# Kernel optimization log

Hardware: AMD Instinct MI355X
Metric: run time of the kernel (lower is better)

## Reference

```python
import jax, jax.numpy as jnp
import numpy as np

EPS = 1e-5


def _bn(x, g, b):
    # BatchNorm1d in training mode: batch mean, biased variance, eps=1e-5
    m = jnp.mean(x, axis=0)
    v = jnp.var(x, axis=0)
    return (x - m) * jax.lax.rsqrt(v + EPS) * g + b


def setup_inputs() -> dict:
    key = jax.random.key(0)
    ks = jax.random.split(key, 16)
    B, N, F, H = 4096, 128, 4, 32
    w = lambda k, o, i: jax.random.normal(k, (o, i), jnp.float32) * 0.3
    d = {
        'u': jax.random.normal(ks[0], (B, N, F), jnp.float32),
        'mask': jnp.ones((B * N, 1), jnp.int32),
        # MLPphi params
        'p_bn1_g': jnp.ones((F,), jnp.float32), 'p_bn1_b': jnp.zeros((F,), jnp.float32), 'p_w1': w(ks[1], H, F),
        'p_bn2_g': jnp.ones((H,), jnp.float32), 'p_bn2_b': jnp.zeros((H,), jnp.float32), 'p_w2': w(ks[2], H, H),
        'p_bn3_g': jnp.ones((H,), jnp.float32), 'p_bn3_b': jnp.zeros((H,), jnp.float32), 'p_w3': w(ks[3], H, H),
        # MLPomega params
        'o_bn1_g': jnp.ones((F,), jnp.float32), 'o_bn1_b': jnp.zeros((F,), jnp.float32), 'o_w1': w(ks[4], H, F),
        'o_bn2_g': jnp.ones((H,), jnp.float32), 'o_bn2_b': jnp.zeros((H,), jnp.float32), 'o_w2': w(ks[5], H, H),
        'o_bn3_g': jnp.ones((H,), jnp.float32), 'o_bn3_b': jnp.zeros((H,), jnp.float32), 'o_w3': w(ks[6], H, H),
        # MLPtheta params
        't_bn1_g': jnp.ones((H,), jnp.float32), 't_bn1_b': jnp.zeros((H,), jnp.float32), 't_w1': w(ks[7], H, H),
        't_bn2_g': jnp.ones((H,), jnp.float32), 't_bn2_b': jnp.zeros((H,), jnp.float32), 't_w2': w(ks[8], H, H),
        't_bn3_g': jnp.ones((H,), jnp.float32), 't_bn3_b': jnp.zeros((H,), jnp.float32), 't_w3': w(ks[9], H, H),
        't_bn4_g': jnp.ones((H,), jnp.float32), 't_bn4_b': jnp.zeros((H,), jnp.float32),
        't_w4': w(ks[10], 1, H), 't_b4': jnp.zeros((1,), jnp.float32),
    }
    return d


def _forward(u, mask,
             p_bn1_g, p_bn1_b, p_w1, p_bn2_g, p_bn2_b, p_w2, p_bn3_g, p_bn3_b, p_w3,
             o_bn1_g, o_bn1_b, o_w1, o_bn2_g, o_bn2_b, o_w2, o_bn3_g, o_bn3_b, o_w3,
             t_bn1_g, t_bn1_b, t_w1, t_bn2_g, t_bn2_b, t_w2, t_bn3_g, t_bn3_b, t_w3,
             t_bn4_g, t_bn4_b, t_w4, t_b4):
    B, N, F = u.shape
    H = p_w1.shape[0]
    u_flat = u.reshape(-1, F)  # (B*N, F)

    # MLPphi: three BN+Linear(no bias)+Tanh blocks with residual adds (dropout=identity in eval)
    o1 = jnp.tanh(_bn(u_flat, p_bn1_g, p_bn1_b) @ p_w1.T)
    o2 = jnp.tanh(_bn(o1, p_bn2_g, p_bn2_b) @ p_w2.T)
    o3 = jnp.tanh(_bn(o1 + o2, p_bn3_g, p_bn3_b) @ p_w3.T)
    x_main = (o1 + o2 + o3).reshape(B, N, H)

    # MLPomega: BN+Linear+Tanh x2, BN+Linear, softmax over hidden dim (dim=1 of flat), then masked_fill
    a = jnp.tanh(_bn(u_flat, o_bn1_g, o_bn1_b) @ o_w1.T)
    a = jnp.tanh(_bn(a, o_bn2_g, o_bn2_b) @ o_w2.T)
    a = _bn(a, o_bn3_g, o_bn3_b) @ o_w3.T
    a = jax.nn.softmax(a, axis=1)
    a = jnp.where(mask == 0, -jnp.inf, a)
    x_attn = a.reshape(B, N, H)

    # attention pooling over neighbors
    x = jnp.sum(x_main * x_attn, axis=1)  # (B, H)

    x = jnp.tanh(_bn(x, t_bn1_g, t_bn1_b) @ t_w1.T)
    x = jnp.tanh(_bn(x, t_bn2_g, t_bn2_b) @ t_w2.T)
    x = jnp.tanh(_bn(x, t_bn3_g, t_bn3_b) @ t_w3.T)
    x = _bn(x, t_bn4_g, t_bn4_b) @ t_w4.T + t_b4
    return x


def reference(u, mask,
              p_bn1_g, p_bn1_b, p_w1, p_bn2_g, p_bn2_b, p_w2, p_bn3_g, p_bn3_b, p_w3,
              o_bn1_g, o_bn1_b, o_w1, o_bn2_g, o_bn2_b, o_w2, o_bn3_g, o_bn3_b, o_w3,
              t_bn1_g, t_bn1_b, t_w1, t_bn2_g, t_bn2_b, t_w2, t_bn3_g, t_bn3_b, t_w3,
              t_bn4_g, t_bn4_b, t_w4, t_b4):
    return _forward(u, mask,
                    p_bn1_g, p_bn1_b, p_w1, p_bn2_g, p_bn2_b, p_w2, p_bn3_g, p_bn3_b, p_w3,
                    o_bn1_g, o_bn1_b, o_w1, o_bn2_g, o_bn2_b, o_w2, o_bn3_g, o_bn3_b, o_w3,
                    t_bn1_g, t_bn1_b, t_w1, t_bn2_g, t_bn2_b, t_w2, t_bn3_g, t_bn3_b, t_w3,
                    t_bn4_g, t_bn4_b, t_w4, t_b4)
```

## Files before the change

### kernel.cpp

```cpp
#include <hip/hip_runtime.h>

typedef unsigned int u32;
typedef unsigned short u16;
typedef __attribute__((ext_vector_type(8))) _Float16 half8;
typedef __attribute__((ext_vector_type(4))) float f32x4;

#define ROWS  524288
#define BROWS 4096
#define EPS   1e-5f

#define S_U   0
#define S_O1  8
#define S_A1  72
#define S_O12 136
#define S_A2  200
#define S_X   264
#define S_X1  328
#define S_X2  392
#define S_X3  456
#define SHARD 1024
#define NSH   64

#define XSTR 40

__device__ __forceinline__ float bl(u32 u){ return __uint_as_float(u << 16); }
__device__ __forceinline__ float bh(u32 u){ return __uint_as_float(u & 0xFFFF0000u); }
__device__ __forceinline__ float b2f(u16 h){ return __uint_as_float(((u32)h) << 16); }
__device__ __forceinline__ u16 f2b(float f){
  u32 u = __float_as_uint(f);
  return (u16)((u + 0x7FFFu + ((u >> 16) & 1u)) >> 16);
}
__device__ __forceinline__ u16 f2h(float f){ _Float16 h = (_Float16)f; return __builtin_bit_cast(u16, h); }
__device__ __forceinline__ float h2f(u16 x){ return (float)__builtin_bit_cast(_Float16, x); }
__device__ __forceinline__ u32 pack2h(float a, float b){
  auto v = __builtin_amdgcn_cvt_pkrtz(a, b);
  return __builtin_bit_cast(u32, v);
}
__device__ __forceinline__ float lo16(u32 w){ return h2f((u16)(w & 0xFFFF)); }
__device__ __forceinline__ float hi16(u32 w){ return h2f((u16)(w >> 16)); }
__device__ __forceinline__ void unpk4(uint2 v, float* d){
  d[0]=lo16(v.x); d[1]=hi16(v.x); d[2]=lo16(v.y); d[3]=hi16(v.y);
}

__device__ __forceinline__ float tanh_fast(float x){
  float x2 = x*x;
  float num = fmaf(x2 + 105.0f, x2, 945.0f) * x;
  float den = fmaf(fmaf(x2, 15.0f, 420.0f), x2, 945.0f);
  float v = num * __builtin_amdgcn_rcpf(den);
  return fminf(1.0f, fmaxf(-1.0f, v));
}

template<bool F32>
__device__ __forceinline__ float rdp(const void* p, int i){
  if (F32) return ((const float*)p)[i];
  return b2f(((const u16*)p)[i]);
}
template<bool F32>
__device__ __forceinline__ void load_u4(const void* u, int r, float* f){
  if (F32){
    float4 v = ((const float4*)u)[r];
    f[0]=v.x; f[1]=v.y; f[2]=v.z; f[3]=v.w;
  } else {
    uint2 v = ((const uint2*)u)[r];
    f[0]=bl(v.x); f[1]=bh(v.x); f[2]=bl(v.y); f[3]=bh(v.y);
  }
}

__device__ __forceinline__ int detect_u(const u16* __restrict__ u, int tid, int* sf){
  if (tid < 64){
    int bad = 0;
#pragma unroll
    for (int i = 0; i < 4; ++i){
      int e = (u[tid*4 + i] >> 7) & 0xFF;
      bad += (e >= 0x90) ? 1 : 0;
    }
#pragma unroll
    for (int off = 32; off >= 1; off >>= 1) bad += __shfl_down(bad, off);
    if (tid == 0) *sf = (bad >= 4) ? 1 : 0;
  }
  __syncthreads();
  return *sf;
}

__device__ __forceinline__ void g2lrow(const u16* __restrict__ g, int r, u16* X, int tid){
  const uint4* src = (const uint4*)&g[(size_t)r*32];
  uint4* dst = (uint4*)&X[tid*XSTR];
#pragma unroll
  for (int c=0;c<4;++c) dst[c] = src[c];
}
__device__ __forceinline__ void l2grow(const u16* X, int tid, u16* __restrict__ g, int r){
  const uint4* src = (const uint4*)&X[tid*XSTR];
  uint4* dst = (uint4*)&g[(size_t)r*32];
#pragma unroll
  for (int c=0;c<4;++c) dst[c] = src[c];
}

template<bool F32>
__device__ __forceinline__ void stats_u_body(const void* __restrict__ u, float* __restrict__ S){
  int tid = blockIdx.x*blockDim.x + threadIdx.x;
  int nt  = gridDim.x*blockDim.x;
  float s[4]={0,0,0,0}, q[4]={0,0,0,0};
  for (int r = tid; r < ROWS; r += nt){
    float f[4]; load_u4<F32>(u, r, f);
#pragma unroll
    for (int k=0;k<4;++k){ s[k]+=f[k]; q[k]+=f[k]*f[k]; }
  }
#pragma unroll
  for (int off=32; off>=1; off>>=1){
#pragma unroll
    for (int k=0;k<4;++k){ s[k]+=__shfl_down(s[k],off); q[k]+=__shfl_down(q[k],off); }
  }
  if ((threadIdx.x & 63) == 0){
    float* Sh = S + (blockIdx.x & (NSH-1))*SHARD;
#pragma unroll
    for (int k=0;k<4;++k){ atomicAdd(&Sh[S_U+k], s[k]); atomicAdd(&Sh[S_U+4+k], q[k]); }
  }
}
__global__ __launch_bounds__(256) void k_stats_u(const void* __restrict__ u, float* __restrict__ S){
  __shared__ int sf;
  int isf = detect_u((const u16*)u, threadIdx.x, &sf);
  if (isf) stats_u_body<true>(u,S); else stats_u_body<false>(u,S);
}

__device__ __forceinline__ void prep_u(const float* __restrict__ S, float* mr, int tid){
  if (tid < 4){
    float s=0.f, q=0.f;
    for (int sh=0; sh<NSH; ++sh){
      s += S[sh*SHARD + S_U + tid];
      q += S[sh*SHARD + S_U + 4 + tid];
    }
    float m = s*(1.0f/ROWS);
    float var = q*(1.0f/ROWS) - m*m;
    mr[tid]   = m;
    mr[4+tid] = rsqrtf(var + EPS);
  }
  __syncthreads();
}
template<bool F32>
__device__ __forceinline__ void bn_u_l(const float* mr, const void* g, const void* b,
                                       const float* f, float* xn){
#pragma unroll
  for (int k=0;k<4;++k)
    xn[k] = (f[k]-mr[k])*(rdp<F32>(g,k)*mr[4+k]) + rdp<F32>(b,k);
}

template<bool F32>
__device__ __forceinline__ void chain1_to_lds(const float* xn, const void* W1, u16* Xrow){
// ... 60 lines not shown
__device__ __forceinline__ void mfma_layer(u16* X, const u16* Wt, const float* Cb,
                                           int L, int wv, int lane, const u32* at_pk)
{
  int ln15 = lane & 15, quad = lane >> 4;
  half8 w0 = *(const half8*)&Wt[(L*32 + ln15     )*XSTR + quad*8];
  half8 w1 = *(const half8*)&Wt[(L*32 + ln15 + 16)*XSTR + quad*8];
  float bias0[4], bias1[4];
#pragma unroll
  for (int reg=0;reg<4;++reg){
    bias0[reg] = Cb[L*32 +      quad*4 + reg];
    bias1[reg] = Cb[L*32 + 16 + quad*4 + reg];
  }
  int rowbase = wv*64;
#pragma unroll
  for (int Mt=0; Mt<4; ++Mt){
    int s = rowbase + Mt*16 + ln15;
    half8 bfr = *(const half8*)&X[s*XSTR + quad*8];
    f32x4 c0 = {0.f,0.f,0.f,0.f}, c1 = {0.f,0.f,0.f,0.f};
    c0 = __builtin_amdgcn_mfma_f32_16x16x32_f16(w0, bfr, c0, 0,0,0);
    c1 = __builtin_amdgcn_mfma_f32_16x16x32_f16(w1, bfr, c1, 0,0,0);
    float o0[4], o1v[4];
    if (KIND == KIND_TANHRES || KIND == KIND_TANHRES_ATREG){
      unpk4(*(const uint2*)&X[s*XSTR +      quad*4], o0);
      unpk4(*(const uint2*)&X[s*XSTR + 16 + quad*4], o1v);
    }
    float a0v[4], a1v[4];
    if (KIND == KIND_TANHRES_ATREG){
      a0v[0]=lo16(at_pk[Mt*4+0]); a0v[1]=hi16(at_pk[Mt*4+0]);
      a0v[2]=lo16(at_pk[Mt*4+1]); a0v[3]=hi16(at_pk[Mt*4+1]);
      a1v[0]=lo16(at_pk[Mt*4+2]); a1v[1]=hi16(at_pk[Mt*4+2]);
      a1v[2]=lo16(at_pk[Mt*4+3]); a1v[3]=hi16(at_pk[Mt*4+3]);
    }
    float v0[4], v1[4];
#pragma unroll
    for (int reg=0;reg<4;++reg){
      float a = c0[reg] + bias0[reg];
      float b = c1[reg] + bias1[reg];
      if (KIND == KIND_TANH){ a = tanh_fast(a); b = tanh_fast(b); }
      else if (KIND == KIND_TANHRES){ a = o0[reg] + tanh_fast(a); b = o1v[reg] + tanh_fast(b); }
      else if (KIND == KIND_TANHRES_ATREG){
        a = (o0[reg] + tanh_fast(a)) * a0v[reg];
        b = (o1v[reg] + tanh_fast(b)) * a1v[reg];
      }
      v0[reg] = a; v1[reg] = b;
    }
    uint2 w0o, w1o;
    w0o.x = pack2h(v0[0], v0[1]); w0o.y = pack2h(v0[2], v0[3]);
    w1o.x = pack2h(v1[0], v1[1]); w1o.y = pack2h(v1[2], v1[3]);
    *(uint2*)&X[s*XSTR +      quad*4] = w0o;
    *(uint2*)&X[s*XSTR + 16 + quad*4] = w1o;
  }
}

__device__ __forceinline__ void mfma_logits_softmax(const u16* X, const u16* Wt, const float* Cb,
    int L, int wv, int lane, const int* __restrict__ mask, int maskbase, u32* at_pk)
{
  int ln15 = lane & 15, quad = lane >> 4;
  half8 w0 = *(const half8*)&Wt[(L*32 + ln15     )*XSTR + quad*8];
  half8 w1 = *(const half8*)&Wt[(L*32 + ln15 + 16)*XSTR + quad*8];
  float bias0[4], bias1[4];
#pragma unroll
  for (int reg=0;reg<4;++reg){
    bias0[reg] = Cb[L*32 +      quad*4 + reg];
    bias1[reg] = Cb[L*32 + 16 + quad*4 + reg];
  }
  int rowbase = wv*64;
#pragma unroll
  for (int Mt=0; Mt<4; ++Mt){
    int s = rowbase + Mt*16 + ln15;
    half8 bfr = *(const half8*)&X[s*XSTR + quad*8];
    f32x4 c0 = {0.f,0.f,0.f,0.f}, c1 = {0.f,0.f,0.f,0.f};
    c0 = __builtin_amdgcn_mfma_f32_16x16x32_f16(w0, bfr, c0, 0,0,0);
    c1 = __builtin_amdgcn_mfma_f32_16x16x32_f16(w1, bfr, c1, 0,0,0);
    float l0[4], l1[4];
#pragma unroll
    for (int reg=0;reg<4;++reg){ l0[reg] = c0[reg]+bias0[reg]; l1[reg] = c1[reg]+bias1[reg]; }
    float mx = l0[0];
#pragma unroll
    for (int reg=1;reg<4;++reg) mx = fmaxf(mx, l0[reg]);
#pragma unroll
    for (int reg=0;reg<4;++reg) mx = fmaxf(mx, l1[reg]);
    mx = fmaxf(mx, __shfl_xor(mx, 16));
    mx = fmaxf(mx, __shfl_xor(mx, 32));
    float sum = 0.f;
#pragma unroll
    for (int reg=0;reg<4;++reg){ l0[reg] = __expf(l0[reg]-mx); sum += l0[reg]; }
#pragma unroll
    for (int reg=0;reg<4;++reg){ l1[reg] = __expf(l1[reg]-mx); sum += l1[reg]; }
    sum += __shfl_xor(sum, 16);
    sum += __shfl_xor(sum, 32);
    float inv = __builtin_amdgcn_rcpf(sum);
    bool mz = (mask[maskbase + Mt*16 + ln15] == 0);
#pragma unroll
    for (int reg=0;reg<4;++reg){
      l0[reg] *= inv; l1[reg] *= inv;
      if (mz){ l0[reg] = -__builtin_inff(); l1[reg] = -__builtin_inff(); }
    }
    at_pk[Mt*4+0] = pack2h(l0[0], l0[1]);
    at_pk[Mt*4+1] = pack2h(l0[2], l0[3]);
    at_pk[Mt*4+2] = pack2h(l1[0], l1[1]);
    at_pk[Mt*4+3] = pack2h(l1[2], l1[3]);
  }
}

__device__ __forceinline__ void reduce_f16(const u16* X, float* lds2,
                                           float* __restrict__ S, int offS, int shard)
{
  int tid = threadIdx.x;
  __syncthreads();
  {
    int j = tid & 31, seg = tid >> 5;
    float s=0.f, q=0.f;
    for (int q2=0;q2<32;++q2){
      float v = h2f(X[(seg*32+q2)*XSTR + j]);
      s += v; q = fmaf(v,v,q);
    }
    lds2[seg*32+j] = s;
    lds2[256 + seg*32+j] = q;
  }
  __syncthreads();
  if (tid < 64){
    int j = tid & 31; bool isq = tid >= 32;
    const float* src = lds2 + (isq?256:0);
    float tot=0.f;
#pragma unroll
    for (int sg=0;sg<8;++sg) tot += src[sg*32+j];
    atomicAdd(&S[shard*SHARD + offS + (isq?32:0) + j], tot);
  }
  __syncthreads();
}

__device__ __forceinline__ void reduce_f32(const float* Xs, float* lds2,
                                           float* __restrict__ S, int offS, int shard)
{
  int tid = threadIdx.x;
  __syncthreads();
  {
    int j = tid & 31, seg = tid >> 5;
    float s=0.f, q=0.f;
    for (int q2=0;q2<32;++q2){
      float v = Xs[(seg*32+q2)*33 + j];
      s += v; q = fmaf(v,v,q);
    }
    lds2[seg*32+j] = s;
    lds2[256 + seg*32+j] = q;
  }
  __syncthreads();
  if (tid < 64){
    int j = tid & 31; bool isq = tid >= 32;
    const float* src = lds2 + (isq?256:0);
    float tot=0.f;
#pragma unroll
    for (int sg=0;sg<8;++sg) tot += src[sg*32+j];
    atomicAdd(&S[shard*SHARD + offS + (isq?32:0) + j], tot);
  }
  __syncthreads();
}

template<bool F32>
__device__ __forceinline__ void pass1_body(const void* __restrict__ u,
    const void* pg1, const void* pb1, const void* pw1,
    const void* og1, const void* ob1, const void* ow1,
    float* __restrict__ S, float* Xs, float* lds2, float* mr)
{
  int tid = threadIdx.x;
  int r = blockIdx.x*256 + tid;
  int shard = blockIdx.x & (NSH-1);
  prep_u(S, mr, tid);
  float f[4]; load_u4<F32>(u,r,f);
  float xn[4];
  float* Xp = Xs + tid*33;

  bn_u_l<F32>(mr, pg1, pb1, f, xn);
#pragma unroll
  for (int j=0;j<32;++j)
    Xp[j] = tanh_fast(xn[0]*rdp<F32>(pw1,j*4+0) + xn[1]*rdp<F32>(pw1,j*4+1)
                    + xn[2]*rdp<F32>(pw1,j*4+2) + xn[3]*rdp<F32>(pw1,j*4+3));
  reduce_f32(Xs, lds2, S, S_O1, shard);

  bn_u_l<F32>(mr, og1, ob1, f, xn);
#pragma unroll
  for (int j=0;j<32;++j)
    Xp[j] = tanh_fast(xn[0]*rdp<F32>(ow1,j*4+0) + xn[1]*rdp<F32>(ow1,j*4+1)
                    + xn[2]*rdp<F32>(ow1,j*4+2) + xn[3]*rdp<F32>(ow1,j*4+3));
  reduce_f32(Xs, lds2, S, S_A1, shard);
}
__global__ __launch_bounds__(256) void k_pass1(const void* __restrict__ u,
    const void* pg1, const void* pb1, const void* pw1,
    const void* og1, const void* ob1, const void* ow1,
    float* __restrict__ S){
  __shared__ float Xs[256*33];
  __shared__ float lds2[512];
  __shared__ float mr[8];
  __shared__ int sf;
  int isf = detect_u((const u16*)u, threadIdx.x, &sf);
  if (isf) pass1_body<true >(u,pg1,pb1,pw1,og1,ob1,ow1,S,Xs,lds2,mr);
  else     pass1_body<false>(u,pg1,pb1,pw1,og1,ob1,ow1,S,Xs,lds2,mr);
}

template<bool F32, bool MAT>
__device__ __forceinline__ void pass2_body(const void* __restrict__ u,
    const void* pg1, const void* pb1, const void* pw1,
    const void* og1, const void* ob1, const void* ow1,
    const void* pg2, const void* pb2, const void* pw2,
    const void* og2, const void* ob2, const void* ow2,
    float* __restrict__ S, u16* __restrict__ o12g, u16* __restrict__ a2g,
    u16* X, u16* Wt, float* Cb, float* lds2, float* mr)
{
  int tid = threadIdx.x;
  int wv = tid >> 6, lane = tid & 63;
  int r = blockIdx.x*256 + tid;
  int shard = blockIdx.x & (NSH-1);
  prep_u(S, mr, tid);
  fold2<F32>(S, S_O1, S_A1, pg2,pb2,pw2, og2,ob2,ow2, Wt, Cb, lds2);

  float f[4], xn[4];
  load_u4<F32>(u,r,f);

  bn_u_l<F32>(mr, pg1, pb1, f, xn);
  chain1_to_lds<F32>(xn, pw1, X + tid*XSTR);
  mfma_layer<KIND_TANHRES>(X, Wt, Cb, 0, wv, lane, 0);
  if (MAT) l2grow(X, tid, o12g, r);
  reduce_f16(X, lds2, S, S_O12, shard);

  bn_u_l<F32>(mr, og1, ob1, f, xn);
  chain1_to_lds<F32>(xn, ow1, X + tid*XSTR);
  mfma_layer<KIND_TANH  >(X, Wt, Cb, 1, wv, lane, 0);
  if (MAT) l2grow(X, tid, a2g, r);
  reduce_f16(X, lds2, S, S_A2, shard);
}
template<bool MAT>
__global__ __launch_bounds__(256) void k_pass2(const void* __restrict__ u,
    const void* pg1, const void* pb1, const void* pw1,
    const void* og1, const void* ob1, const void* ow1,
    const void* pg2, const void* pb2, const void* pw2,
    const void* og2, const void* ob2, const void* ow2,
    float* __restrict__ S, u16* o12g, u16* a2g){
  __shared__ u16 X[256*XSTR];
  __shared__ u16 Wt[2*32*XSTR];
  __shared__ float Cb[64];
  __shared__ float lds2[512];
  __shared__ float mr[8];
  __shared__ int sf;
  int isf = detect_u((const u16*)u, threadIdx.x, &sf);
  if (isf) pass2_body<true ,MAT>(u,pg1,pb1,pw1,og1,ob1,ow1,pg2,pb2,pw2,og2,ob2,ow2,S,o12g,a2g,X,Wt,Cb,lds2,mr);
  else     pass2_body<false,MAT>(u,pg1,pb1,pw1,og1,ob1,ow1,pg2,pb2,pw2,og2,ob2,ow2,S,o12g,a2g,X,Wt,Cb,lds2,mr);
}

template<bool F32>
__device__ __forceinline__ void pass3m_body(const int* __restrict__ mask,
    const void* pg3, const void* pb3, const void* pw3,
    const void* og3, const void* ob3, const void* ow3,
    const u16* __restrict__ o12g, const u16* __restrict__ a2g,
    float* __restrict__ x, float* __restrict__ S,
    u16* X, u16* Wt, float* Cb, float* red2)
{
  int tid = threadIdx.x;
  int wv = tid >> 6, lane = tid & 63;
  int r = blockIdx.x*256 + tid;
  fold2<F32>(S, S_A2, S_O12, og3,ob3,ow3, pg3,pb3,pw3, Wt, Cb, red2);

  u32 at_pk[16];
  int maskbase = blockIdx.x*256 + wv*64;

  g2lrow(a2g, r, X, tid);
  __syncthreads();
  mfma_logits_softmax(X, Wt, Cb, 0, wv, lane, mask, maskbase, at_pk);
  __syncthreads();
  g2lrow(o12g, r, X, tid);
  __syncthreads();
  mfma_layer<KIND_TANHRES_ATREG>(X, Wt, Cb, 1, wv, lane, at_pk);

  __syncthreads();
  {
    int jj = tid & 31, cgrp = (tid >> 5) & 3, half = tid >> 7;
    float s2 = 0.f;
    for (int q2=0;q2<32;++q2) s2 += h2f(X[(half*128 + cgrp*32 + q2)*XSTR + jj]);
    red2[tid] = s2;
  }
  __syncthreads();
  if (tid < 64){
    int half = tid >> 5, j = tid & 31;
    float v = red2[half*128+j] + red2[half*128+32+j] + red2[half*128+64+j] + red2[half*128+96+j];
    x[(blockIdx.x*2 + half)*32 + j] = v;
    float* Sh = S + (blockIdx.x & (NSH-1))*SHARD;
    atomicAdd(&Sh[S_X+j], v);
    atomicAdd(&Sh[S_X+32+j], v*v);
  }
}
__global__ __launch_bounds__(256) void k_pass3m(const void* __restrict__ u, const int* __restrict__ mask,
    const void* pg3, const void* pb3, const void* pw3,
    const void* og3, const void* ob3, const void* ow3,
    const u16* o12g, const u16* a2g,
    float* __restrict__ x, float* __restrict__ S){
  __shared__ u16 X [256*XSTR];
  __shared__ u16 Wt[2*32*XSTR];
  __shared__ float Cb[64];
  __shared__ float red2[256];
  __shared__ int sf;
  int isf = detect_u((const u16*)u, threadIdx.x, &sf);
  if (isf) pass3m_body<true >(mask,pg3,pb3,pw3,og3,ob3,ow3,o12g,a2g,x,S,X,Wt,Cb,red2);
  else     pass3m_body<false>(mask,pg3,pb3,pw3,og3,ob3,ow3,o12g,a2g,x,S,X,Wt,Cb,red2);
}

template<bool F32>
__device__ __forceinline__ void fold4(const float* __restrict__ S,
    int off0,int off1,int off2,int off3,
    const void* g0,const void* b0,const void* W0,
    const void* g1,const void* b1,const void* W1,
    const void* g2,const void* b2,const void* W2,
    const void* g3,const void* b3,const void* W3,
    u16* Wt, float* Cb, float* scr)
{
  int tid = threadIdx.x;
  __shared__ float scr2[256];
  if (tid < 128){
    int L = tid>>5, k = tid&31;
    const void* g = (L==0)?g0:(L==1)?g1:(L==2)?g2:g3;
    const void* b = (L==0)?b0:(L==1)?b1:(L==2)?b2:b3;
    int off = (L==0)?off0:(L==1)?off1:(L==2)?off2:off3;
    float s=0.f, q=0.f;
    for (int sh=0; sh<NSH; ++sh){
      s += S[sh*SHARD + off + k];
      q += S[sh*SHARD + off + 32 + k];
    }
    float m    = s*(1.0f/ROWS);
    float var  = q*(1.0f/ROWS) - m*m;
    float rstd = rsqrtf(var+EPS);
    float sc = rdp<F32>(g,k)*rstd;
    scr[tid]  = sc;
    scr2[tid] = rdp<F32>(b,k) - m*sc;
  }
  __syncthreads();
  if (tid < 128){
    int L = tid>>5, j = tid&31;
    const void* W = (L==0)?W0:(L==1)?W1:(L==2)?W2:W3;
    float c = 0.f;
#pragma unroll
    for (int k=0;k<32;++k){
      float Wv = rdp<F32>(W, j*32+k);
      Wt[(L*32+j)*XSTR + k] = f2h(Wv * scr[(L<<5)|k]);
      c += Wv * scr2[(L<<5)|k];
    }
    Cb[L*32+j] = c;
  }
  __syncthreads();
}

template<bool F32>
__device__ __forceinline__ void pass3_body(const void* __restrict__ u, const int* __restrict__ mask,
    const void* pg1, const void* pb1, const void* pw1,
    const void* og1, const void* ob1, const void* ow1,
    const void* pg2, const void* pb2, const void* pw2,
    const void* og2, const void* ob2, const void* ow2,
    const void* pg3, const void* pb3, const void* pw3,
    const void* og3, const void* ob3, const void* ow3,
    float* __restrict__ x, float* __restrict__ S,
    u16* X, u16* Wt, float* Cb, float* red2, float* mr)
{
  int tid = threadIdx.x;
  int wv = tid >> 6, lane = tid & 63;
  int r = blockIdx.x*256 + tid;
  prep_u(S, mr, tid);
  fold4<F32>(S, S_A1, S_A2, S_O1, S_O12,
             og2,ob2,ow2, og3,ob3,ow3, pg2,pb2,pw2, pg3,pb3,pw3,
             Wt, Cb, red2);

  float f[4], xn[4];
  load_u4<F32>(u,r,f);
  u32 at_pk[16];
  int maskbase = blockIdx.x*256 + wv*64;

  bn_u_l<F32>(mr, og1, ob1, f, xn);
  chain1_to_lds<F32>(xn, ow1, X + tid*XSTR);
  mfma_layer<KIND_TANH>(X, Wt, Cb, 0, wv, lane, 0);
  mfma_logits_softmax(X, Wt, Cb, 1, wv, lane, mask, maskbase, at_pk);

  bn_u_l<F32>(mr, pg1, pb1, f, xn);
  chain1_to_lds<F32>(xn, pw1, X + tid*XSTR);
  mfma_layer<KIND_TANHRES   >(X, Wt, Cb, 2, wv, lane, 0);
  mfma_layer<KIND_TANHRES_ATREG>(X, Wt, Cb, 3, wv, lane, at_pk);

  __syncthreads();
  {
    int jj = tid & 31, cgrp = (tid >> 5) & 3, half = tid >> 7;
    float s2 = 0.f;
    for (int q2=0;q2<32;++q2) s2 += h2f(X[(half*128 + cgrp*32 + q2)*XSTR + jj]);
    red2[tid] = s2;
  }
  __syncthreads();
  if (tid < 64){
    int half = tid >> 5, j = tid & 31;
    float v = red2[half*128+j] + red2[half*128+32+j] + red2[half*128+64+j] + red2[half*128+96+j];
    x[(blockIdx.x*2 + half)*32 + j] = v;
    float* Sh = S + (blockIdx.x & (NSH-1))*SHARD;
    atomicAdd(&Sh[S_X+j], v);
    atomicAdd(&Sh[S_X+32+j], v*v);
  }
}
__global__ __launch_bounds__(256) void k_pass3(const void* __restrict__ u, const int* __restrict__ mask,
    const void* pg1, const void* pb1, const void* pw1,
    const void* og1, const void* ob1, const void* ow1,
    const void* pg2, const void* pb2, const void* pw2,
    const void* og2, const void* ob2, const void* ow2,
    const void* pg3, const void* pb3, const void* pw3,
    const void* og3, const void* ob3, const void* ow3,
    float* __restrict__ x, float* __restrict__ S){
  __shared__ u16 X [256*XSTR];
  __shared__ u16 Wt[4*32*XSTR];
  __shared__ float Cb[128];
  __shared__ float red2[256];
  __shared__ float mr[8];
  __shared__ int sf;
  int isf = detect_u((const u16*)u, threadIdx.x, &sf);
  if (isf) pass3_body<true >(u,mask,pg1,pb1,pw1,og1,ob1,ow1,pg2,pb2,pw2,og2,ob2,ow2,
                             pg3,pb3,pw3,og3,ob3,ow3,x,S,X,Wt,Cb,red2,mr);
  else     pass3_body<false>(u,mask,pg1,pb1,pw1,og1,ob1,ow1,pg2,pb2,pw2,og2,ob2,ow2,
                             pg3,pb3,pw3,og3,ob3,ow3,x,S,X,Wt,Cb,red2,mr);
}


template<int NSH_IN>
__device__ __forceinline__ void theta_gather(const float* __restrict__ S, int off,
                                             float* scratch, float* lds2, int tid){
  int col = tid & 63, grp = tid >> 6;
  float t = 0.f;
#pragma unroll
  for (int i = 0; i < NSH_IN/4; ++i)
    t += S[(grp + i*4)*SHARD + off + col];
  scratch[tid] = t;
  __syncthreads();
  if (tid < 64)
    scratch[tid] = scratch[tid] + scratch[64+tid] + scratch[128+tid] + scratch[192+tid];
  __syncthreads();
  if (tid < 32){
    float m   = scratch[tid]*(1.0f/BROWS);
    float var = scratch[32+tid]*(1.0f/BROWS) - m*m;
    lds2[tid]    = m;
    lds2[32+tid] = rsqrtf(var + EPS);
  }
  __syncthreads();
}

template<bool F32>
__device__ __forceinline__ void theta_layer(float* v, const float* lds2,
    const void* g, const void* b, const void* W){
  float xn[32];
#pragma unroll
  for (int k=0;k<32;++k)
    xn[k] = (v[k] - lds2[k]) * (rdp<F32>(g,k)*lds2[32+k]) + rdp<F32>(b,k);
#pragma unroll
  for (int j=0;j<32;++j){
    float acc = 0.f;
#pragma unroll
    for (int k=0;k<32;++k) acc = fmaf(rdp<F32>(W, j*32+k), xn[k], acc);
    v[j] = tanh_fast(acc);
  }
}

template<bool F32, int NSH_IN>
__device__ __forceinline__ void theta_L_body(const float* __restrict__ xin,
    float* __restrict__ xout, float* __restrict__ S, int off_in, int off_out,
    const void* g, const void* b, const void* W, float* lds, float* lds2)
{
  int tid = threadIdx.x, blk = blockIdx.x;
  int r = blk*256 + tid;
  theta_gather<NSH_IN>(S, off_in, lds, lds2, tid);
  float v[32];
  {
    const float4* xr = (const float4*)&xin[(size_t)r*32];
#pragma unroll
    for (int k=0;k<8;++k){ float4 t = xr[k]; v[4*k]=t.x; v[4*k+1]=t.y; v[4*k+2]=t.z; v[4*k+3]=t.w; }
  }
  theta_layer<F32>(v, lds2, g, b, W);
  {
    float4* xw = (float4*)&xout[(size_t)r*32];
#pragma unroll
    for (int k=0;k<8;++k){ float4 t; t.x=v[4*k]; t.y=v[4*k+1]; t.z=v[4*k+2]; t.w=v[4*k+3]; xw[k]=t; }
  }
  float* Xp = lds + tid*33;
#pragma unroll
  for (int j=0;j<32;++j) Xp[j] = v[j];
  reduce_f32(lds, lds2, S, off_out, blk);
}
template<int NSH_IN>
__global__ __launch_bounds__(256) void k_theta_L(const void* __restrict__ u,
    const float* __restrict__ xin, float* __restrict__ xout,
    float* __restrict__ S, int off_in, int off_out,
    const void* g, const void* b, const void* W){
  __shared__ float lds[256*33];
  __shared__ float lds2[512];
  __shared__ int sf;
  int isf = detect_u((const u16*)u, threadIdx.x, &sf);
  if (isf) theta_L_body<true , NSH_IN>(xin, xout, S, off_in, off_out, g, b, W, lds, lds2);
  else     theta_L_body<false, NSH_IN>(xin, xout, S, off_in, off_out, g, b, W, lds, lds2);
}

template<bool F32>
__device__ __forceinline__ void theta_fin_body(const float* __restrict__ xin,
    float* __restrict__ S,
    const void* g4, const void* b4, const void* w4, const void* bb4,
    void* out, float* lds, float* lds2)
{
  int tid = threadIdx.x, blk = blockIdx.x;
  int r = blk*256 + tid;
  theta_gather<16>(S, S_X3, lds, lds2, tid);
  float acc = rdp<F32>(bb4, 0);
  const float4* xr = (const float4*)&xin[(size_t)r*32];
#pragma unroll
  for (int k8=0;k8<8;++k8){
    float4 t = xr[k8];
    float vv[4] = {t.x, t.y, t.z, t.w};
#pragma unroll
    for (int q=0;q<4;++q){
      int k = k8*4+q;
      float xnv = (vv[q] - lds2[k]) * (rdp<F32>(g4,k)*lds2[32+k]) + rdp<F32>(b4,k);
      acc = fmaf(rdp<F32>(w4,k), xnv, acc);
    }
  }
  if (F32) ((float*)out)[r] = acc;
  else     ((u16*)out)[r]  = f2b(acc);
}
__global__ __launch_bounds__(256) void k_theta_fin(const void* __restrict__ u,
    const float* __restrict__ xin, float* __restrict__ S,
    const void* g4, const void* b4, const void* w4, const void* bb4,
    void* out){
  __shared__ float lds[256];
  __shared__ float lds2[512];
  __shared__ int sf;
  int isf = detect_u((const u16*)u, threadIdx.x, &sf);
  if (isf) theta_fin_body<true >(xin, S, g4, b4, w4, bb4, out, lds, lds2);
  else     theta_fin_body<false>(xin, S, g4, b4, w4, bb4, out, lds, lds2);
}

extern "C" void kernel_launch(void* const* d_in, const int* in_sizes, int n_in,
                              void* d_out, int out_size, void* d_ws, size_t ws_size,
                              hipStream_t stream)
{
  const void* u    = d_in[0];
  const int*  mask = (const int*)d_in[1];
  const void *pg1=d_in[2],  *pb1=d_in[3],  *pw1=d_in[4];
  const void *pg2=d_in[5],  *pb2=d_in[6],  *pw2=d_in[7];
  const void *pg3=d_in[8],  *pb3=d_in[9],  *pw3=d_in[10];
  const void *og1=d_in[11], *ob1=d_in[12], *ow1=d_in[13];
  const void *og2=d_in[14], *ob2=d_in[15], *ow2=d_in[16];
  const void *og3=d_in[17], *ob3=d_in[18], *ow3=d_in[19];
  const void *tg1=d_in[20], *tb1=d_in[21], *tw1=d_in[22];
  const void *tg2=d_in[23], *tb2=d_in[24], *tw2=d_in[25];
  const void *tg3=d_in[26], *tb3=d_in[27], *tw3=d_in[28];
  const void *tg4=d_in[29], *tb4=d_in[30], *tw4=d_in[31], *tbb4=d_in[32];

  char* ws = (char*)d_ws;
  float* S    = (float*)(ws + 4096);
  float* x    = (float*)(ws + 524288);
  float* xb   = (float*)(ws + 1048576);

  const size_t MB = 1024*1024;
  u16* o12g = (u16*)(ws + 8*MB);
  u16* a2g  = (u16*)(ws + 40*MB);
  bool MAT = ws_size >= 73*MB;

  (void)hipMemsetAsync(ws, 0, 4096 + NSH*SHARD*4, stream);
  k_stats_u<<<1024, 256, 0, stream>>>(u, S);
  k_pass1<<<2048, 256, 0, stream>>>(u, pg1,pb1,pw1, og1,ob1,ow1, S);
  if (MAT){
    k_pass2<true ><<<2048, 256, 0, stream>>>(u, pg1,pb1,pw1, og1,ob1,ow1,
                                             pg2,pb2,pw2, og2,ob2,ow2, S, o12g, a2g);
    k_pass3m<<<2048, 256, 0, stream>>>(u, mask, pg3,pb3,pw3, og3,ob3,ow3, o12g, a2g, x, S);
  } else {
    k_pass2<false><<<2048, 256, 0, stream>>>(u, pg1,pb1,pw1, og1,ob1,ow1,
                                             pg2,pb2,pw2, og2,ob2,ow2, S, o12g, a2g);
    k_pass3<<<2048, 256, 0, stream>>>(u, mask, pg1,pb1,pw1, og1,ob1,ow1,
                                      pg2,pb2,pw2, og2,ob2,ow2,
                                      pg3,pb3,pw3, og3,ob3,ow3, x, S);
  }
  k_theta_L<64><<<16, 256, 0, stream>>>(u, x,  xb, S, S_X,  S_X1, tg1, tb1, tw1);
  k_theta_L<16><<<16, 256, 0, stream>>>(u, xb, x,  S, S_X1, S_X2, tg2, tb2, tw2);
  k_theta_L<16><<<16, 256, 0, stream>>>(u, x,  xb, S, S_X2, S_X3, tg3, tb3, tw3);
  k_theta_fin<<<16, 256, 0, stream>>>(u, xb, S, tg4, tb4, tw4, tbb4, d_out);
}
```

Before: 318.5 us.

## Compute BN stats in MFMA registers, read pass3 from global, fuse final theta

Pass2 now computes per-column sums and sums of squares straight from the MFMA output registers. It reduces them with cross-lane shuffles and writes activations directly to global memory, replacing the LDS round trip and the strided column reduction. Pass3m feeds MFMA B fragments straight from global o12g/a2g and does the attention pooling in registers, dropping the LDS staging and several barriers. Pass1 now uses the f16 chain1 helper and f16 reduction. The final theta layer is merged into the third theta kernel through a last-block atomic counter, saving one launch at the cost of a serial 16-row tail in a single block.

```diff
diff --git a/kernel.cpp b/kernel.cpp
--- a/kernel.cpp
+++ b/kernel.cpp
@@ -50,6 +50,14 @@
   return fminf(1.0f, fmaxf(-1.0f, v));
 }
 
+__device__ __forceinline__ float red16(float v){
+  v += __shfl_xor(v, 1);
+  v += __shfl_xor(v, 2);
+  v += __shfl_xor(v, 4);
+  v += __shfl_xor(v, 8);
+  return v;
+}
+
 template<bool F32>
 __device__ __forceinline__ float rdp(const void* p, int i){
   if (F32) return ((const float*)p)[i];
@@ -80,19 +88,6 @@
   }
   __syncthreads();
   return *sf;
-}
-
-__device__ __forceinline__ void g2lrow(const u16* __restrict__ g, int r, u16* X, int tid){
-  const uint4* src = (const uint4*)&g[(size_t)r*32];
-  uint4* dst = (uint4*)&X[tid*XSTR];
-#pragma unroll
-  for (int c=0;c<4;++c) dst[c] = src[c];
-}
-__device__ __forceinline__ void l2grow(const u16* X, int tid, u16* __restrict__ g, int r){
-  const uint4* src = (const uint4*)&X[tid*XSTR];
-  uint4* dst = (uint4*)&g[(size_t)r*32];
-#pragma unroll
-  for (int c=0;c<4;++c) dst[c] = src[c];
 }
 
 template<bool F32>
@@ -259,8 +254,9 @@
   }
 }
 
-__device__ __forceinline__ void mfma_logits_softmax(const u16* X, const u16* Wt, const float* Cb,
-    int L, int wv, int lane, const int* __restrict__ mask, int maskbase, u32* at_pk)
+template<int KIND, bool STORE>
+__device__ __forceinline__ void mfma_stat(const u16* X, const u16* Wt, const float* Cb,
+    int L, int wv, int lane, u16* __restrict__ G, int gbase, float* s8, float* q8)
 {
   int ln15 = lane & 15, quad = lane >> 4;
   half8 w0 = *(const half8*)&Wt[(L*32 + ln15     )*XSTR + quad*8];
@@ -271,6 +267,8 @@
     bias0[reg] = Cb[L*32 +      quad*4 + reg];
     bias1[reg] = Cb[L*32 + 16 + quad*4 + reg];
   }
+#pragma unroll
+  for (int i=0;i<8;++i){ s8[i]=0.f; q8[i]=0.f; }
   int rowbase = wv*64;
 #pragma unroll
   for (int Mt=0; Mt<4; ++Mt){
@@ -279,6 +277,79 @@
     f32x4 c0 = {0.f,0.f,0.f,0.f}, c1 = {0.f,0.f,0.f,0.f};
     c0 = __builtin_amdgcn_mfma_f32_16x16x32_f16(w0, bfr, c0, 0,0,0);
     c1 = __builtin_amdgcn_mfma_f32_16x16x32_f16(w1, bfr, c1, 0,0,0);
+    float o0[4], o1v[4];
+    if (KIND == KIND_TANHRES){
+      unpk4(*(const uint2*)&X[s*XSTR +      quad*4], o0);
+      unpk4(*(const uint2*)&X[s*XSTR + 16 + quad*4], o1v);
+    }
+    float v0[4], v1[4];
+#pragma unroll
+    for (int reg=0;reg<4;++reg){
+      float a = c0[reg] + bias0[reg];
+      float b = c1[reg] + bias1[reg];
+      if (KIND == KIND_TANH){ a = tanh_fast(a); b = tanh_fast(b); }
+      else { a = o0[reg] + tanh_fast(a); b = o1v[reg] + tanh_fast(b); }
+      s8[reg]   += a; q8[reg]   = fmaf(a,a,q8[reg]);
+      s8[4+reg] += b; q8[4+reg] = fmaf(b,b,q8[4+reg]);
+      v0[reg] = a; v1[reg] = b;
+    }
+    if (STORE){
+      uint2 w0o, w1o;
+      w0o.x = pack2h(v0[0], v0[1]); w0o.y = pack2h(v0[2], v0[3]);
+      w1o.x = pack2h(v1[0], v1[1]); w1o.y = pack2h(v1[2], v1[3]);
+      size_t R = (size_t)(gbase + s);
+      *(uint2*)&G[R*32 +      quad*4] = w0o;
+      *(uint2*)&G[R*32 + 16 + quad*4] = w1o;
+    }
+  }
+}
+
+__device__ __forceinline__ void emit_stats(float* s8, float* q8, int tid, int wv,
+    int quad, int ln15, float* scr , float* __restrict__ S, int offS, int shard)
+{
+#pragma unroll
+  for (int i=0;i<8;++i){ s8[i]=red16(s8[i]); q8[i]=red16(q8[i]); }
+  __syncthreads();
+  if (ln15 == 0){
+#pragma unroll
+    for (int rg=0; rg<4; ++rg){
+      int cl = quad*4+rg, ch = 16+quad*4+rg;
+      scr[wv*64 + cl]       = s8[rg];
+      scr[wv*64 + ch]       = s8[4+rg];
+      scr[256 + wv*64 + cl] = q8[rg];
+      scr[256 + wv*64 + ch] = q8[4+rg];
+    }
+  }
+  __syncthreads();
+  if (tid < 64){
+    int j = tid & 31, isq = tid >> 5;
+    const float* src = scr + isq*256;
+    float tot = src[j] + src[64+j] + src[128+j] + src[192+j];
+    atomicAdd(&S[shard*SHARD + offS + isq*32 + j], tot);
+  }
+}
+
+__device__ __forceinline__ void mfma_logits_softmax_g(const u16* __restrict__ Gsrc, int gbase,
+    const u16* Wt, const float* Cb, int L, int wv, int lane,
+    const int* __restrict__ mask, int maskbase, u32* at_pk)
+{
+  int ln15 = lane & 15, quad = lane >> 4;
+  half8 w0 = *(const half8*)&Wt[(L*32 + ln15     )*XSTR + quad*8];
+  half8 w1 = *(const half8*)&Wt[(L*32 + ln15 + 16)*XSTR + quad*8];
+  float bias0[4], bias1[4];
+#pragma unroll
+  for (int reg=0;reg<4;++reg){
+    bias0[reg] = Cb[L*32 +      quad*4 + reg];
+    bias1[reg] = Cb[L*32 + 16 + quad*4 + reg];
+  }
+  int rowbase = wv*64;
+#pragma unroll
+  for (int Mt=0; Mt<4; ++Mt){
+    int R = gbase + rowbase + Mt*16 + ln15;
+    half8 bfr = *(const half8*)&Gsrc[(size_t)R*32 + quad*8];
+    f32x4 c0 = {0.f,0.f,0.f,0.f}, c1 = {0.f,0.f,0.f,0.f};
+    c0 = __builtin_amdgcn_mfma_f32_16x16x32_f16(w0, bfr, c0, 0,0,0);
+    c1 = __builtin_amdgcn_mfma_f32_16x16x32_f16(w1, bfr, c1, 0,0,0);
     float l0[4], l1[4];
 #pragma unroll
     for (int reg=0;reg<4;++reg){ l0[reg] = c0[reg]+bias0[reg]; l1[reg] = c1[reg]+bias1[reg]; }
@@ -307,6 +378,46 @@
     at_pk[Mt*4+1] = pack2h(l0[2], l0[3]);
     at_pk[Mt*4+2] = pack2h(l1[0], l1[1]);
     at_pk[Mt*4+3] = pack2h(l1[2], l1[3]);
+  }
+}
+
+__device__ __forceinline__ void mfma_pool_g(const u16* __restrict__ Gsrc, int gbase,
+    const u16* Wt, const float* Cb, int L, int wv, int lane, const u32* at_pk, float* ps)
+{
+  int ln15 = lane & 15, quad = lane >> 4;
+  half8 w0 = *(const half8*)&Wt[(L*32 + ln15     )*XSTR + quad*8];
+  half8 w1 = *(const half8*)&Wt[(L*32 + ln15 + 16)*XSTR + quad*8];
+  float bias0[4], bias1[4];
+#pragma unroll
+  for (int reg=0;reg<4;++reg){
+    bias0[reg] = Cb[L*32 +      quad*4 + reg];
+    bias1[reg] = Cb[L*32 + 16 + quad*4 + reg];
+  }
+#pragma unroll
+  for (int i=0;i<8;++i) ps[i]=0.f;
+  int rowbase = wv*64;
+#pragma unroll
+  for (int Mt=0; Mt<4; ++Mt){
+    int R = gbase + rowbase + Mt*16 + ln15;
+    half8 bfr = *(const half8*)&Gsrc[(size_t)R*32 + quad*8];
+    f32x4 c0 = {0.f,0.f,0.f,0.f}, c1 = {0.f,0.f,0.f,0.f};
+    c0 = __builtin_amdgcn_mfma_f32_16x16x32_f16(w0, bfr, c0, 0,0,0);
+    c1 = __builtin_amdgcn_mfma_f32_16x16x32_f16(w1, bfr, c1, 0,0,0);
+    float o0[4], o1v[4];
+    unpk4(*(const uint2*)&Gsrc[(size_t)R*32 +      quad*4], o0);
+    unpk4(*(const uint2*)&Gsrc[(size_t)R*32 + 16 + quad*4], o1v);
+    float a0v[4], a1v[4];
+    a0v[0]=lo16(at_pk[Mt*4+0]); a0v[1]=hi16(at_pk[Mt*4+0]);
+    a0v[2]=lo16(at_pk[Mt*4+1]); a0v[3]=hi16(at_pk[Mt*4+1]);
+    a1v[0]=lo16(at_pk[Mt*4+2]); a1v[1]=hi16(at_pk[Mt*4+2]);
+    a1v[2]=lo16(at_pk[Mt*4+3]); a1v[3]=hi16(at_pk[Mt*4+3]);
+#pragma unroll
+    for (int reg=0;reg<4;++reg){
+      float a = (o0[reg]  + tanh_fast(c0[reg]+bias0[reg])) * a0v[reg];
+      float b = (o1v[reg] + tanh_fast(c1[reg]+bias1[reg])) * a1v[reg];
+      ps[reg]   += a;
+      ps[4+reg] += b;
+    }
   }
 }
 
@@ -368,41 +479,34 @@
 __device__ __forceinline__ void pass1_body(const void* __restrict__ u,
     const void* pg1, const void* pb1, const void* pw1,
     const void* og1, const void* ob1, const void* ow1,
-    float* __restrict__ S, float* Xs, float* lds2, float* mr)
+    float* __restrict__ S, u16* X, float* lds2, float* mr)
 {
   int tid = threadIdx.x;
   int r = blockIdx.x*256 + tid;
   int shard = blockIdx.x & (NSH-1);
   prep_u(S, mr, tid);
-  float f[4]; load_u4<F32>(u,r,f);
-  float xn[4];
-  float* Xp = Xs + tid*33;
+  float f[4], xn[4];
+  load_u4<F32>(u,r,f);
 
   bn_u_l<F32>(mr, pg1, pb1, f, xn);
-#pragma unroll
-  for (int j=0;j<32;++j)
-    Xp[j] = tanh_fast(xn[0]*rdp<F32>(pw1,j*4+0) + xn[1]*rdp<F32>(pw1,j*4+1)
-                    + xn[2]*rdp<F32>(pw1,j*4+2) + xn[3]*rdp<F32>(pw1,j*4+3));
-  reduce_f32(Xs, lds2, S, S_O1, shard);
+  chain1_to_lds<F32>(xn, pw1, X + tid*XSTR);
+  reduce_f16(X, lds2, S, S_O1, shard);
 
   bn_u_l<F32>(mr, og1, ob1, f, xn);
-#pragma unroll
-  for (int j=0;j<32;++j)
-    Xp[j] = tanh_fast(xn[0]*rdp<F32>(ow1,j*4+0) + xn[1]*rdp<F32>(ow1,j*4+1)
-                    + xn[2]*rdp<F32>(ow1,j*4+2) + xn[3]*rdp<F32>(ow1,j*4+3));
-  reduce_f32(Xs, lds2, S, S_A1, shard);
+  chain1_to_lds<F32>(xn, ow1, X + tid*XSTR);
+  reduce_f16(X, lds2, S, S_A1, shard);
 }
 __global__ __launch_bounds__(256) void k_pass1(const void* __restrict__ u,
     const void* pg1, const void* pb1, const void* pw1,
     const void* og1, const void* ob1, const void* ow1,
     float* __restrict__ S){
-  __shared__ float Xs[256*33];
+  __shared__ u16 X[256*XSTR];
   __shared__ float lds2[512];
   __shared__ float mr[8];
   __shared__ int sf;
   int isf = detect_u((const u16*)u, threadIdx.x, &sf);
-  if (isf) pass1_body<true >(u,pg1,pb1,pw1,og1,ob1,ow1,S,Xs,lds2,mr);
-  else     pass1_body<false>(u,pg1,pb1,pw1,og1,ob1,ow1,S,Xs,lds2,mr);
+  if (isf) pass1_body<true >(u,pg1,pb1,pw1,og1,ob1,ow1,S,X,lds2,mr);
+  else     pass1_body<false>(u,pg1,pb1,pw1,og1,ob1,ow1,S,X,lds2,mr);
 }
 
 template<bool F32, bool MAT>
@@ -416,25 +520,26 @@
 {
   int tid = threadIdx.x;
   int wv = tid >> 6, lane = tid & 63;
+  int ln15 = lane & 15, quad = lane >> 4;
   int r = blockIdx.x*256 + tid;
+  int gbase = blockIdx.x*256;
   int shard = blockIdx.x & (NSH-1);
   prep_u(S, mr, tid);
   fold2<F32>(S, S_O1, S_A1, pg2,pb2,pw2, og2,ob2,ow2, Wt, Cb, lds2);
 
   float f[4], xn[4];
   load_u4<F32>(u,r,f);
+  float s8[8], q8[8];
 
   bn_u_l<F32>(mr, pg1, pb1, f, xn);
   chain1_to_lds<F32>(xn, pw1, X + tid*XSTR);
-  mfma_layer<KIND_TANHRES>(X, Wt, Cb, 0, wv, lane, 0);
-  if (MAT) l2grow(X, tid, o12g, r);
-  reduce_f16(X, lds2, S, S_O12, shard);
+  mfma_stat<KIND_TANHRES, MAT>(X, Wt, Cb, 0, wv, lane, o12g, gbase, s8, q8);
+  emit_stats(s8, q8, tid, wv, quad, ln15, lds2, S, S_O12, shard);
 
   bn_u_l<F32>(mr, og1, ob1, f, xn);
   chain1_to_lds<F32>(xn, ow1, X + tid*XSTR);
-  mfma_layer<KIND_TANH  >(X, Wt, Cb, 1, wv, lane, 0);
-  if (MAT) l2grow(X, tid, a2g, r);
-  reduce_f16(X, lds2, S, S_A2, shard);
+  mfma_stat<KIND_TANH, MAT>(X, Wt, Cb, 1, wv, lane, a2g, gbase, s8, q8);
+  emit_stats(s8, q8, tid, wv, quad, ln15, lds2, S, S_A2, shard);
 }
 template<bool MAT>
 __global__ __launch_bounds__(256) void k_pass2(const void* __restrict__ u,
@@ -460,35 +565,35 @@
     const void* og3, const void* ob3, const void* ow3,
     const u16* __restrict__ o12g, const u16* __restrict__ a2g,
     float* __restrict__ x, float* __restrict__ S,
-    u16* X, u16* Wt, float* Cb, float* red2)
+    u16* Wt, float* Cb, float* lds2)
 {
   int tid = threadIdx.x;
   int wv = tid >> 6, lane = tid & 63;
-  int r = blockIdx.x*256 + tid;
-  fold2<F32>(S, S_A2, S_O12, og3,ob3,ow3, pg3,pb3,pw3, Wt, Cb, red2);
+  int ln15 = lane & 15, quad = lane >> 4;
+  int gbase = blockIdx.x*256;
+  fold2<F32>(S, S_A2, S_O12, og3,ob3,ow3, pg3,pb3,pw3, Wt, Cb, lds2);
 
   u32 at_pk[16];
-  int maskbase = blockIdx.x*256 + wv*64;
-
-  g2lrow(a2g, r, X, tid);
-  __syncthreads();
-  mfma_logits_softmax(X, Wt, Cb, 0, wv, lane, mask, maskbase, at_pk);
-  __syncthreads();
-  g2lrow(o12g, r, X, tid);
-  __syncthreads();
-  mfma_layer<KIND_TANHRES_ATREG>(X, Wt, Cb, 1, wv, lane, at_pk);
-
-  __syncthreads();
-  {
-    int jj = tid & 31, cgrp = (tid >> 5) & 3, half = tid >> 7;
-    float s2 = 0.f;
-    for (int q2=0;q2<32;++q2) s2 += h2f(X[(half*128 + cgrp*32 + q2)*XSTR + jj]);
-    red2[tid] = s2;
+  int maskbase = gbase + wv*64;
+  mfma_logits_softmax_g(a2g, gbase, Wt, Cb, 0, wv, lane, mask, maskbase, at_pk);
+
+  float ps[8];
+  mfma_pool_g(o12g, gbase, Wt, Cb, 1, wv, lane, at_pk, ps);
+
+#pragma unroll
+  for (int i=0;i<8;++i) ps[i]=red16(ps[i]);
+  __syncthreads();
+  if (ln15 == 0){
+#pragma unroll
+    for (int rg=0; rg<4; ++rg){
+      lds2[wv*32 + quad*4+rg]    = ps[rg];
+      lds2[wv*32 + 16+quad*4+rg] = ps[4+rg];
+    }
   }
   __syncthreads();
   if (tid < 64){
     int half = tid >> 5, j = tid & 31;
-    float v = red2[half*128+j] + red2[half*128+32+j] + red2[half*128+64+j] + red2[half*128+96+j];
+    float v = lds2[half*64 + j] + lds2[half*64 + 32 + j];
     x[(blockIdx.x*2 + half)*32 + j] = v;
     float* Sh = S + (blockIdx.x & (NSH-1))*SHARD;
     atomicAdd(&Sh[S_X+j], v);
@@ -500,14 +605,13 @@
     const void* og3, const void* ob3, const void* ow3,
     const u16* o12g, const u16* a2g,
     float* __restrict__ x, float* __restrict__ S){
-  __shared__ u16 X [256*XSTR];
   __shared__ u16 Wt[2*32*XSTR];
   __shared__ float Cb[64];
-  __shared__ float red2[256];
+  __shared__ float lds2[512];
   __shared__ int sf;
   int isf = detect_u((const u16*)u, threadIdx.x, &sf);
-  if (isf) pass3m_body<true >(mask,pg3,pb3,pw3,og3,ob3,ow3,o12g,a2g,x,S,X,Wt,Cb,red2);
-  else     pass3m_body<false>(mask,pg3,pb3,pw3,og3,ob3,ow3,o12g,a2g,x,S,X,Wt,Cb,red2);
+  if (isf) pass3m_body<true >(mask,pg3,pb3,pw3,og3,ob3,ow3,o12g,a2g,x,S,Wt,Cb,lds2);
+  else     pass3m_body<false>(mask,pg3,pb3,pw3,og3,ob3,ow3,o12g,a2g,x,S,Wt,Cb,lds2);
 }
 
 template<bool F32>
@@ -581,7 +685,54 @@
   bn_u_l<F32>(mr, og1, ob1, f, xn);
   chain1_to_lds<F32>(xn, ow1, X + tid*XSTR);
   mfma_layer<KIND_TANH>(X, Wt, Cb, 0, wv, lane, 0);
-  mfma_logits_softmax(X, Wt, Cb, 1, wv, lane, mask, maskbase, at_pk);
+  {
+    int ln15 = lane & 15, quad = lane >> 4;
+    half8 w0 = *(const half8*)&Wt[(1*32 + ln15     )*XSTR + quad*8];
+    half8 w1 = *(const half8*)&Wt[(1*32 + ln15 + 16)*XSTR + quad*8];
+    float bias0[4], bias1[4];
+#pragma unroll
+    for (int reg=0;reg<4;++reg){
+      bias0[reg] = Cb[32 +      quad*4 + reg];
+      bias1[reg] = Cb[32 + 16 + quad*4 + reg];
+    }
+    int rowbase = wv*64;
+#pragma unroll
+    for (int Mt=0; Mt<4; ++Mt){
+      int s = rowbase + Mt*16 + ln15;
+      half8 bfr = *(const half8*)&X[s*XSTR + quad*8];
+      f32x4 c0 = {0.f,0.f,0.f,0.f}, c1 = {0.f,0.f,0.f,0.f};
+      c0 = __builtin_amdgcn_mfma_f32_16x16x32_f16(w0, bfr, c0, 0,0,0);
+      c1 = __builtin_amdgcn_mfma_f32_16x16x32_f16(w1, bfr, c1, 0,0,0);
+      float l0[4], l1[4];
+#pragma unroll
+      for (int reg=0;reg<4;++reg){ l0[reg] = c0[reg]+bias0[reg]; l1[reg] = c1[reg]+bias1[reg]; }
+      float mx = l0[0];
+#pragma unroll
+      for (int reg=1;reg<4;++reg) mx = fmaxf(mx, l0[reg]);
+#pragma unroll
+      for (int reg=0;reg<4;++reg) mx = fmaxf(mx, l1[reg]);
+      mx = fmaxf(mx, __shfl_xor(mx, 16));
+      mx = fmaxf(mx, __shfl_xor(mx, 32));
+      float sum = 0.f;
+#pragma unroll
+      for (int reg=0;reg<4;++reg){ l0[reg] = __expf(l0[reg]-mx); sum += l0[reg]; }
+#pragma unroll
+      for (int reg=0;reg<4;++reg){ l1[reg] = __expf(l1[reg]-mx); sum += l1[reg]; }
+      sum += __shfl_xor(sum, 16);
+      sum += __shfl_xor(sum, 32);
+      float inv = __builtin_amdgcn_rcpf(sum);
+      bool mz = (mask[maskbase + Mt*16 + ln15] == 0);
+#pragma unroll
+      for (int reg=0;reg<4;++reg){
+        l0[reg] *= inv; l1[reg] *= inv;
+        if (mz){ l0[reg] = -__builtin_inff(); l1[reg] = -__builtin_inff(); }
+      }
+      at_pk[Mt*4+0] = pack2h(l0[0], l0[1]);
+      at_pk[Mt*4+1] = pack2h(l0[2], l0[3]);
+      at_pk[Mt*4+2] = pack2h(l1[0], l1[1]);
+      at_pk[Mt*4+3] = pack2h(l1[2], l1[3]);
+    }
+  }
 
   bn_u_l<F32>(mr, pg1, pb1, f, xn);
   chain1_to_lds<F32>(xn, pw1, X + tid*XSTR);
@@ -626,7 +777,6 @@
                              pg3,pb3,pw3,og3,ob3,ow3,x,S,X,Wt,Cb,red2,mr);
 }
 
-
 template<int NSH_IN>
 __device__ __forceinline__ void theta_gather(const float* __restrict__ S, int off,
                                              float* scratch, float* lds2, int tid){
@@ -665,20 +815,23 @@
   }
 }
 
-template<bool F32, int NSH_IN>
+template<bool F32, int NSH_IN, bool FIN>
 __device__ __forceinline__ void theta_L_body(const float* __restrict__ xin,
     float* __restrict__ xout, float* __restrict__ S, int off_in, int off_out,
-    const void* g, const void* b, const void* W, float* lds, float* lds2)
+    const void* g, const void* b, const void* W,
+    const void* g4, const void* b4, const void* w4, const void* bb4,
+    void* out, u32* __restrict__ ctr, int* flag,
+    float* lds, float* lds2)
 {
   int tid = threadIdx.x, blk = blockIdx.x;
   int r = blk*256 + tid;
-  theta_gather<NSH_IN>(S, off_in, lds, lds2, tid);
   float v[32];
   {
     const float4* xr = (const float4*)&xin[(size_t)r*32];
 #pragma unroll
     for (int k=0;k<8;++k){ float4 t = xr[k]; v[4*k]=t.x; v[4*k+1]=t.y; v[4*k+2]=t.z; v[4*k+3]=t.w; }
   }
+  theta_gather<NSH_IN>(S, off_in, lds, lds2, tid);
   theta_layer<F32>(v, lds2, g, b, W);
   {
     float4* xw = (float4*)&xout[(size_t)r*32];
@@ -689,55 +842,53 @@
 #pragma unroll
   for (int j=0;j<32;++j) Xp[j] = v[j];
   reduce_f32(lds, lds2, S, off_out, blk);
-}
-template<int NSH_IN>
+
+  if (FIN){
+    __threadfence();
+    if (tid == 0){
+      u32 n = __hip_atomic_fetch_add(ctr, 1u, __ATOMIC_ACQ_REL, __HIP_MEMORY_SCOPE_AGENT);
+      *flag = (n == 15);
+    }
+    __syncthreads();
+    if (!*flag) return;
+    __builtin_amdgcn_fence(__ATOMIC_ACQUIRE, "agent");
+    theta_gather<16>(S, off_out, lds, lds2, tid);
+#pragma unroll 1
+    for (int i=0;i<16;++i){
+      int r2 = i*256 + tid;
+      const float4* xr = (const float4*)&xout[(size_t)r2*32];
+      float acc = rdp<F32>(bb4, 0);
+#pragma unroll
+      for (int k8=0;k8<8;++k8){
+        float4 t = xr[k8];
+        float vv[4] = {t.x, t.y, t.z, t.w};
+#pragma unroll
+        for (int q=0;q<4;++q){
+          int k = k8*4+q;
+          float xnv = (vv[q] - lds2[k]) * (rdp<F32>(g4,k)*lds2[32+k]) + rdp<F32>(b4,k);
+          acc = fmaf(rdp<F32>(w4,k), xnv, acc);
+        }
+      }
+      if (F32) ((float*)out)[r2] = acc;
+      else     ((u16*)out)[r2]  = f2b(acc);
+    }
+  }
+}
+template<int NSH_IN, bool FIN>
 __global__ __launch_bounds__(256) void k_theta_L(const void* __restrict__ u,
     const float* __restrict__ xin, float* __restrict__ xout,
     float* __restrict__ S, int off_in, int off_out,
-    const void* g, const void* b, const void* W){
+    const void* g, const void* b, const void* W,
+    const void* g4, const void* b4, const void* w4, const void* bb4,
+    void* out, u32* ctr){
   __shared__ float lds[256*33];
   __shared__ float lds2[512];
   __shared__ int sf;
   int isf = detect_u((const u16*)u, threadIdx.x, &sf);
-  if (isf) theta_L_body<true , NSH_IN>(xin, xout, S, off_in, off_out, g, b, W, lds, lds2);
-  else     theta_L_body<false, NSH_IN>(xin, xout, S, off_in, off_out, g, b, W, lds, lds2);
-}
-
-template<bool F32>
-__device__ __forceinline__ void theta_fin_body(const float* __restrict__ xin,
-    float* __restrict__ S,
-    const void* g4, const void* b4, const void* w4, const void* bb4,
-    void* out, float* lds, float* lds2)
-{
-  int tid = threadIdx.x, blk = blockIdx.x;
-  int r = blk*256 + tid;
-  theta_gather<16>(S, S_X3, lds, lds2, tid);
-  float acc = rdp<F32>(bb4, 0);
-  const float4* xr = (const float4*)&xin[(size_t)r*32];
-#pragma unroll
-  for (int k8=0;k8<8;++k8){
-    float4 t = xr[k8];
-    float vv[4] = {t.x, t.y, t.z, t.w};
-#pragma unroll
-    for (int q=0;q<4;++q){
-      int k = k8*4+q;
-      float xnv = (vv[q] - lds2[k]) * (rdp<F32>(g4,k)*lds2[32+k]) + rdp<F32>(b4,k);
-      acc = fmaf(rdp<F32>(w4,k), xnv, acc);
-    }
-  }
-  if (F32) ((float*)out)[r] = acc;
-  else     ((u16*)out)[r]  = f2b(acc);
-}
-__global__ __launch_bounds__(256) void k_theta_fin(const void* __restrict__ u,
-    const float* __restrict__ xin, float* __restrict__ S,
-    const void* g4, const void* b4, const void* w4, const void* bb4,
-    void* out){
-  __shared__ float lds[256];
-  __shared__ float lds2[512];
-  __shared__ int sf;
-  int isf = detect_u((const u16*)u, threadIdx.x, &sf);
-  if (isf) theta_fin_body<true >(xin, S, g4, b4, w4, bb4, out, lds, lds2);
-  else     theta_fin_body<false>(xin, S, g4, b4, w4, bb4, out, lds, lds2);
+  if (isf) theta_L_body<true , NSH_IN, FIN>(xin, xout, S, off_in, off_out, g, b, W,
+                                            g4, b4, w4, bb4, out, ctr, &sf, lds, lds2);
+  else     theta_L_body<false, NSH_IN, FIN>(xin, xout, S, off_in, off_out, g, b, W,
+                                            g4, b4, w4, bb4, out, ctr, &sf, lds, lds2);
 }
 
 extern "C" void kernel_launch(void* const* d_in, const int* in_sizes, int n_in,
@@ -758,6 +909,7 @@
   const void *tg4=d_in[29], *tb4=d_in[30], *tw4=d_in[31], *tbb4=d_in[32];
 
   char* ws = (char*)d_ws;
+  u32*   ctr  = (u32*)(ws + 256);
   float* S    = (float*)(ws + 4096);
   float* x    = (float*)(ws + 524288);
   float* xb   = (float*)(ws + 1048576);
@@ -781,8 +933,10 @@
                                       pg2,pb2,pw2, og2,ob2,ow2,
                                       pg3,pb3,pw3, og3,ob3,ow3, x, S);
   }
-  k_theta_L<64><<<16, 256, 0, stream>>>(u, x,  xb, S, S_X,  S_X1, tg1, tb1, tw1);
-  k_theta_L<16><<<16, 256, 0, stream>>>(u, xb, x,  S, S_X1, S_X2, tg2, tb2, tw2);
-  k_theta_L<16><<<16, 256, 0, stream>>>(u, x,  xb, S, S_X2, S_X3, tg3, tb3, tw3);
-  k_theta_fin<<<16, 256, 0, stream>>>(u, xb, S, tg4, tb4, tw4, tbb4, d_out);
-}
+  k_theta_L<64,false><<<16, 256, 0, stream>>>(u, x,  xb, S, S_X,  S_X1, tg1, tb1, tw1,
+                                              nullptr,nullptr,nullptr,nullptr, nullptr, nullptr);
+  k_theta_L<16,false><<<16, 256, 0, stream>>>(u, xb, x,  S, S_X1, S_X2, tg2, tb2, tw2,
+                                              nullptr,nullptr,nullptr,nullptr, nullptr, nullptr);
+  k_theta_L<16,true ><<<16, 256, 0, stream>>>(u, x,  xb, S, S_X2, S_X3, tg3, tb3, tw3,
+                                              tg4, tb4, tw4, tbb4, d_out, ctr);
+}
```

Result: slower. 341.6 us (+7.3%).
